# Optimization experiments

Hardware: AMD Instinct MI355X
Metric: run time of the kernel (lower is better)

Reference implementation:

```python
import jax, jax.numpy as jnp
import numpy as np

TOKEN_DIM = 256
NUM_HEADS = 2
IN_DIMS = 512
D = TOKEN_DIM * NUM_HEADS  # 512
SCALE = TOKEN_DIM ** (-0.5)


def _l2norm(v, axis):
    # torch F.normalize: v / max(||v||_2, eps)
    n = jnp.sqrt(jnp.sum(v * v, axis=axis, keepdims=True))
    return v / jnp.maximum(n, 1e-12)


def setup_inputs() -> dict:
    key = jax.random.key(0)
    ks = jax.random.split(key, 10)
    b, n = 8, 4096
    x = jax.random.normal(ks[0], (b, n, IN_DIMS), dtype=jnp.float32)
    s = 0.02
    Wq = jax.random.normal(ks[1], (IN_DIMS, D), dtype=jnp.float32) * s
    bq = jax.random.normal(ks[2], (D,), dtype=jnp.float32) * s
    Wk = jax.random.normal(ks[3], (IN_DIMS, D), dtype=jnp.float32) * s
    bk = jax.random.normal(ks[4], (D,), dtype=jnp.float32) * s
    Wr = jax.random.normal(ks[5], (D, TOKEN_DIM), dtype=jnp.float32) * s
    br = jax.random.normal(ks[6], (TOKEN_DIM,), dtype=jnp.float32) * s
    w_alpha = jax.random.normal(ks[7], (D, 1), dtype=jnp.float32)
    w_beta = jax.random.normal(ks[8], (D, 1), dtype=jnp.float32)
    return {"x": x, "Wq": Wq, "bq": bq, "Wk": Wk, "bk": bk,
            "Wr": Wr, "br": br, "w_alpha": w_alpha, "w_beta": w_beta}


def reference(x, Wq, bq, Wk, bk, Wr, br, w_alpha, w_beta):
    # x: [b, n, in_dims]
    q = x @ Wq + bq                      # [b, n, D]
    k = x @ Wk + bk                      # [b, n, D]
    q = _l2norm(q, axis=-1)
    k = _l2norm(k, axis=-1)
    v = _l2norm(k, axis=-1)              # original bug: value = normalize(key)

    alpha_w = (q @ w_alpha) * SCALE      # [b, n, 1]
    alpha_w = _l2norm(alpha_w, axis=1)   # normalize over token axis
    g_q = jnp.sum(alpha_w * q, axis=1)   # [b, D]
    g_q = jax.nn.softmax(g_q, axis=-1)

    p = g_q[:, None, :] * k              # [b, n, D]
    beta_w = _l2norm((p @ w_beta) * SCALE, axis=1)  # [b, n, 1]
    g_k = jnp.sum(beta_w * p, axis=1)    # [b, D]
    g_k = jax.nn.softmax(g_k, axis=-1)

    kvi = g_k[:, None, :] * v + q        # [b, n, D]
    return kvi @ Wr + br                 # [b, n, token_dim]
```

## Files before the change

kernel.cpp:

```cpp
#include <hip/hip_runtime.h>
#include <hip/hip_bf16.h>
#include <stdint.h>

#define BATCH    8
#define NTOKB    4096
#define NTOK     (BATCH * NTOKB)
#define DIN      512
#define DD       512
#define TD       256
#define SCALE    0.0625f
#define LSTR     36

typedef unsigned short ushortT;
typedef __attribute__((ext_vector_type(8))) short  short8;
typedef __attribute__((ext_vector_type(4))) float  f32x4;

union Frag { uint4 u; short8 s; };

__device__ __forceinline__ float bf_lo(uint32_t u) { return __uint_as_float(u << 16); }
__device__ __forceinline__ float bf_hi(uint32_t u) { return __uint_as_float(u & 0xffff0000u); }
__device__ __forceinline__ ushortT f2bf(float f) {
    uint32_t u = __float_as_uint(f);
    return (ushortT)((u + 0x7fffu + ((u >> 16) & 1u)) >> 16);
}
__device__ __forceinline__ short8 lds_frag(const ushortT* p) {
    uint2 a = *reinterpret_cast<const uint2*>(p);
    uint2 b = *reinterpret_cast<const uint2*>(p + 4);
    Frag f; f.u.x = a.x; f.u.y = a.y; f.u.z = b.x; f.u.w = b.y;
    return f.s;
}
__device__ __forceinline__ void gload_lds16(const ushortT* g, ushortT* l) {
    __builtin_amdgcn_global_load_lds(
        (const __attribute__((address_space(1))) uint32_t*)(const void*)g,
        (__attribute__((address_space(3))) uint32_t*)(void*)l,
        16, 0, 0);
}

__global__ __launch_bounds__(256) void packw_kernel(
    const float* __restrict__ Wq, const float* __restrict__ Wk,
    const float* __restrict__ Wr, ushortT* __restrict__ W16)
{
    const int blk = blockIdx.x;
    if (blk < 32) {
        const int mat = blk >> 4, c = blk & 15;
        const float* S = mat ? Wk : Wq;
        ushortT* D = W16 + (size_t)mat * (512 * 512) + (size_t)c * 16384;
        for (int i = threadIdx.x; i < 16384; i += 256) {
            int n = i & 511, p = i >> 9;
            int l = ((p >> 3) ^ ((n >> 1) & 3)) * 8 + (p & 7);
            D[n * 32 + p] = f2bf(S[(size_t)(c * 32 + l) * 512 + n]);
        }
    } else {
        const int c = blk - 32;
        ushortT* D = W16 + (size_t)2 * (512 * 512) + (size_t)c * 8192;
        for (int i = threadIdx.x; i < 8192; i += 256) {
            int n = i & 255, p = i >> 8;
            int l = ((p >> 3) ^ ((n >> 1) & 3)) * 8 + (p & 7);
            D[n * 32 + p] = f2bf(Wr[(size_t)(c * 32 + l) * 256 + n]);
        }
    }
}

__global__ __launch_bounds__(512) void gemm_qk_kernel(
    const float* __restrict__ x, const ushortT* __restrict__ W16,
    const float* __restrict__ bq, const float* __restrict__ bk,
    const float* __restrict__ w_alpha,
    ushortT* __restrict__ qn, ushortT* __restrict__ kn,
    float* __restrict__ alpha_raw, float* __restrict__ gq_raw)
{
    __shared__ __align__(16) ushortT xs[64 * LSTR];
    __shared__ __align__(16) ushortT wsd[512 * 32];
    __shared__ float rowsq[8][64];
    __shared__ float alphap[8][64];
    __shared__ float rnorm_s[64];
    __shared__ float alpha_sh[64];

    const int tid = threadIdx.x;
    const int mat = blockIdx.y;
    const size_t tok0 = (size_t)blockIdx.x * 64;
    const int b = (int)(blockIdx.x >> 6);
    const ushortT* Wb = W16 + (size_t)mat * (512 * 512);
    const float* bias = mat ? bk : bq;
    ushortT* dst = mat ? kn : qn;

    const int lane = tid & 63, w = tid >> 6;
    const int m = lane & 15, quad = lane >> 4;

    f32x4 acc[4][4];
    #pragma unroll
    for (int tr = 0; tr < 4; ++tr)
        #pragma unroll
        for (int tc = 0; tc < 4; ++tc) acc[tr][tc] = (f32x4){0.f, 0.f, 0.f, 0.f};

    const int xtok = tid >> 3;
    const int xkg  = (tid & 7) * 4;
    const float* xsrc = x + (tok0 + xtok) * DIN;

    for (int c = 0; c < 16; ++c) {
        __syncthreads();
        {
            float4 xv = *reinterpret_cast<const float4*>(xsrc + c * 32 + xkg);
            ushort4 xb;
            xb.x = f2bf(xv.x); xb.y = f2bf(xv.y); xb.z = f2bf(xv.z); xb.w = f2bf(xv.w);
            *reinterpret_cast<ushort4*>(&xs[xtok * LSTR + xkg]) = xb;
        }
        {
            const ushortT* wsrc = Wb + (size_t)c * 16384;
            #pragma unroll
            for (int i = 0; i < 4; ++i) {
                const int region = i * 8 + w;
                gload_lds16(wsrc + region * 512 + lane * 8, &wsd[region * 512]);
            }
        }
        __syncthreads();
        {
            short8 af[4], bfv[4];
            #pragma unroll
            for (int tr = 0; tr < 4; ++tr)
                af[tr] = lds_frag(&xs[(tr * 16 + m) * LSTR + quad * 8]);
            #pragma unroll
            for (int tc = 0; tc < 4; ++tc) {
                const int n = w * 64 + tc * 16 + m;
                bfv[tc] = *reinterpret_cast<const short8*>(
                    &wsd[n * 32 + ((quad ^ ((n >> 1) & 3)) * 8)]);
            }
            #pragma unroll
            for (int tr = 0; tr < 4; ++tr)
                #pragma unroll
                for (int tc = 0; tc < 4; ++tc)
                    acc[tr][tc] = __builtin_amdgcn_mfma_f32_16x16x32_bf16(af[tr], bfv[tc], acc[tr][tc], 0, 0, 0);
        }
    }

    float biasv[4], wa[4];
    #pragma unroll
    for (int tc = 0; tc < 4; ++tc) {
        biasv[tc] = bias[w * 64 + tc * 16 + m];
        wa[tc] = (mat == 0) ? w_alpha[w * 64 + tc * 16 + m] : 0.f;
    }
    #pragma unroll
    for (int tr = 0; tr < 4; ++tr)
        #pragma unroll
        for (int tc = 0; tc < 4; ++tc)
            #pragma unroll
            for (int reg = 0; reg < 4; ++reg)
                acc[tr][tc][reg] += biasv[tc];

    __syncthreads();
    #pragma unroll
    for (int tr = 0; tr < 4; ++tr) {
        #pragma unroll
        for (int reg = 0; reg < 4; ++reg) {
            float s = 0.f, a = 0.f;
            #pragma unroll
            for (int tc = 0; tc < 4; ++tc) {
                float v = acc[tr][tc][reg];
                s = fmaf(v, v, s);
                a = fmaf(v, wa[tc], a);
            }
            #pragma unroll
            for (int off = 1; off < 16; off <<= 1) {
                s += __shfl_xor(s, off);
                a += __shfl_xor(a, off);
            }
            if (m == 0) {
                rowsq[w][tr * 16 + quad * 4 + reg] = s;
                alphap[w][tr * 16 + quad * 4 + reg] = a;
            }
        }
    }
    __syncthreads();
    if (tid < 64) {
        float ss = 0.f, aa = 0.f;
        #pragma unroll
        for (int w2 = 0; w2 < 8; ++w2) { ss += rowsq[w2][tid]; aa += alphap[w2][tid]; }
        float rn = 1.0f / fmaxf(sqrtf(ss), 1e-12f);
        float av = SCALE * aa * rn;
        rnorm_s[tid] = rn;
        alpha_sh[tid] = av;
        if (mat == 0) alpha_raw[tok0 + tid] = av;
    }
    __syncthreads();
    float gqp[4] = {0.f, 0.f, 0.f, 0.f};
    #pragma unroll
    for (int tr = 0; tr < 4; ++tr) {
        #pragma unroll
        for (int reg = 0; reg < 4; ++reg) {
            const int rloc = tr * 16 + quad * 4 + reg;
            float rn = rnorm_s[rloc];
            float av = alpha_sh[rloc];
            size_t row = tok0 + rloc;
            ushortT* rp = dst + row * DD + w * 64 + m;
            #pragma unroll
            for (int tc = 0; tc < 4; ++tc) {
                float val = acc[tr][tc][reg] * rn;
                rp[tc * 16] = f2bf(val);
                gqp[tc] = fmaf(av, val, gqp[tc]);
            }
        }
    }
    if (mat == 0) {
        #pragma unroll
        for (int tc = 0; tc < 4; ++tc) {
            float p = gqp[tc];
            p += __shfl_xor(p, 16);
            p += __shfl_xor(p, 32);
            if (quad == 0)
                atomicAdd(&gq_raw[b * DD + w * 64 + tc * 16 + m], p);
        }
    }
}

__global__ __launch_bounds__(256) void fused_softmax_kernel(
    const float* __restrict__ nrm_in, const float* __restrict__ in,
    const float* __restrict__ mul, const float* __restrict__ wbeta,
    float* __restrict__ out, float* __restrict__ wb2)
{
    int b = blockIdx.x, tid = threadIdx.x;
    __shared__ float red[256];
    float s = 0.f;
    for (int i = tid; i < NTOKB; i += 256) {
        float v = nrm_in[b * NTOKB + i];
        s = fmaf(v, v, s);
    }
    red[tid] = s;
    __syncthreads();
    for (int off = 128; off > 0; off >>= 1) {
        if (tid < off) red[tid] += red[tid + off];
        __syncthreads();
    }
    float inv = 1.0f / fmaxf(sqrtf(red[0]), 1e-12f);
    __syncthreads();
    float v0 = in[b * DD + tid] * inv, v1 = in[b * DD + 256 + tid] * inv;
    if (mul) { v0 *= mul[b * DD + tid]; v1 *= mul[b * DD + 256 + tid]; }
    red[tid] = fmaxf(v0, v1);
    __syncthreads();
    for (int off = 128; off > 0; off >>= 1) {
        if (tid < off) red[tid] = fmaxf(red[tid], red[tid + off]);
        __syncthreads();
    }
    float m = red[0];
    __syncthreads();
    float e0 = expf(v0 - m), e1 = expf(v1 - m);
    red[tid] = e0 + e1;
    __syncthreads();
    for (int off = 128; off > 0; off >>= 1) {
        if (tid < off) red[tid] += red[tid + off];
        __syncthreads();
    }
    float rs = 1.0f / red[0];
    float o0 = e0 * rs, o1 = e1 * rs;
    out[b * DD + tid] = o0;
    out[b * DD + 256 + tid] = o1;
    if (wb2) {
        wb2[b * DD + tid]       = o0 * wbeta[tid];
        wb2[b * DD + 256 + tid] = o1 * wbeta[256 + tid];
    }
}

__global__ __launch_bounds__(256) void betawsum_kernel(
    const ushortT* __restrict__ kn, const float* __restrict__ wb2,
    float* __restrict__ beta_raw, float* __restrict__ h_raw)
{
    const int blk = blockIdx.x, tid = threadIdx.x;
    const int b = blk >> 6;
    const int i0 = (blk & 63) * 64;
    __shared__ float bs[64];

    const int wave = tid >> 6, lane = tid & 63;
    float4 wv0 = *reinterpret_cast<const float4*>(wb2 + b * DD + lane * 8);
    float4 wv1 = *reinterpret_cast<const float4*>(wb2 + b * DD + lane * 8 + 4);

    for (int it = 0; it < 16; ++it) {
        const int t = it * 4 + wave;
        const size_t tok = (size_t)b * NTOKB + i0 + t;
        uint4 kv = *reinterpret_cast<const uint4*>(kn + tok * DD + lane * 8);
        float s = bf_lo(kv.x) * wv0.x + bf_hi(kv.x) * wv0.y
                + bf_lo(kv.y) * wv0.z + bf_hi(kv.y) * wv0.w
                + bf_lo(kv.z) * wv1.x + bf_hi(kv.z) * wv1.y
                + bf_lo(kv.w) * wv1.z + bf_hi(kv.w) * wv1.w;
        #pragma unroll
        for (int off = 32; off > 0; off >>= 1) s += __shfl_xor(s, off);
        if (lane == 0) {
            float bv = SCALE * s;
            bs[t] = bv;
            beta_raw[tok] = bv;
        }
    }
    __syncthreads();

    const uint32_t* M32 = reinterpret_cast<const uint32_t*>(kn);
    size_t base = ((size_t)b * NTOKB + i0) * 256 + tid;
    float a0 = 0.f, a1 = 0.f;
    for (int ii = 0; ii < 64; ++ii) {
        uint32_t v = M32[base + (size_t)ii * 256];
        float wv = bs[ii];
        a0 = fmaf(wv, bf_lo(v), a0);
        a1 = fmaf(wv, bf_hi(v), a1);
    }
    atomicAdd(&h_raw[b * DD + 2 * tid],     a0);
    atomicAdd(&h_raw[b * DD + 2 * tid + 1], a1);
}

__global__ __launch_bounds__(256) void out_mfma_kernel(
    const ushortT* __restrict__ qn, const ushortT* __restrict__ kn,
    const float* __restrict__ g_k, const ushortT* __restrict__ WrT,
    const float* __restrict__ br, float* __restrict__ out)
{
    __shared__ __align__(16) ushortT kvs[64 * LSTR];
    __shared__ __align__(16) ushortT wrs[256 * 32];
    __shared__ float gks[512];

    const int tid = threadIdx.x;
    const size_t tok0 = (size_t)blockIdx.x * 64;
    const int b = (int)(tok0 >> 12);

    gks[tid] = g_k[b * DD + tid];
    gks[256 + tid] = g_k[b * DD + 256 + tid];

    const int lane = tid & 63, w = tid >> 6;
    const int m = lane & 15, quad = lane >> 4;

    f32x4 acc[4][4];
    #pragma unroll
    for (int tr = 0; tr < 4; ++tr)
        #pragma unroll
        for (int tc = 0; tc < 4; ++tc) acc[tr][tc] = (f32x4){0.f, 0.f, 0.f, 0.f};

    const int st  = tid >> 2;
    const int skg = (tid & 3) * 8;

    for (int c = 0; c < 16; ++c) {
        __syncthreads();
        {
            const size_t base = (tok0 + st) * DD + c * 32 + skg;
            uint4 qv = *reinterpret_cast<const uint4*>(qn + base);
            uint4 kv = *reinterpret_cast<const uint4*>(kn + base);
            const float* g = &gks[c * 32 + skg];
            ushortT o[8];
            o[0] = f2bf(fmaf(g[0], bf_lo(kv.x), bf_lo(qv.x)));
            o[1] = f2bf(fmaf(g[1], bf_hi(kv.x), bf_hi(qv.x)));
            o[2] = f2bf(fmaf(g[2], bf_lo(kv.y), bf_lo(qv.y)));
            o[3] = f2bf(fmaf(g[3], bf_hi(kv.y), bf_hi(qv.y)));
            o[4] = f2bf(fmaf(g[4], bf_lo(kv.z), bf_lo(qv.z)));
            o[5] = f2bf(fmaf(g[5], bf_hi(kv.z), bf_hi(qv.z)));
            o[6] = f2bf(fmaf(g[6], bf_lo(kv.w), bf_lo(qv.w)));
            o[7] = f2bf(fmaf(g[7], bf_hi(kv.w), bf_hi(qv.w)));
            uint2* lp = reinterpret_cast<uint2*>(&kvs[st * LSTR + skg]);
            lp[0] = make_uint2(((uint32_t)o[1] << 16) | o[0], ((uint32_t)o[3] << 16) | o[2]);
            lp[1] = make_uint2(((uint32_t)o[5] << 16) | o[4], ((uint32_t)o[7] << 16) | o[6]);
        }
        {
            const ushortT* wsrc = WrT + (size_t)c * 8192;
            #pragma unroll
            for (int i = 0; i < 4; ++i) {
                const int region = i * 4 + w;
                gload_lds16(wsrc + region * 512 + lane * 8, &wrs[region * 512]);
            }
        }
        __syncthreads();
        {
            short8 af[4], bfr[4];
            #pragma unroll
            for (int tr = 0; tr < 4; ++tr)
                af[tr] = lds_frag(&kvs[(tr * 16 + m) * LSTR + quad * 8]);
            #pragma unroll
            for (int tc = 0; tc < 4; ++tc) {
                const int n = w * 64 + tc * 16 + m;
                bfr[tc] = *reinterpret_cast<const short8*>(
                    &wrs[n * 32 + ((quad ^ ((n >> 1) & 3)) * 8)]);
            }
            #pragma unroll
            for (int tr = 0; tr < 4; ++tr)
                #pragma unroll
                for (int tc = 0; tc < 4; ++tc)
                    acc[tr][tc] = __builtin_amdgcn_mfma_f32_16x16x32_bf16(af[tr], bfr[tc], acc[tr][tc], 0, 0, 0);
        }
    }

    float brv[4];
    #pragma unroll
    for (int tc = 0; tc < 4; ++tc) brv[tc] = br[w * 64 + tc * 16 + m];
    #pragma unroll
    for (int tr = 0; tr < 4; ++tr) {
        #pragma unroll
        for (int reg = 0; reg < 4; ++reg) {
            size_t row = tok0 + tr * 16 + quad * 4 + reg;
            float* rp = out + row * TD + w * 64 + m;
            #pragma unroll
            for (int tc = 0; tc < 4; ++tc)
                rp[tc * 16] = acc[tr][tc][reg] + brv[tc];
        }
    }
}

extern "C" void kernel_launch(void* const* d_in, const int* in_sizes, int n_in,
                              void* d_out, int out_size, void* d_ws, size_t ws_size,
                              hipStream_t stream)
{
    const float* x       = (const float*)d_in[0];
    const float* Wq      = (const float*)d_in[1];
    const float* bq      = (const float*)d_in[2];
    const float* Wk      = (const float*)d_in[3];
    const float* bk      = (const float*)d_in[4];
    const float* Wr      = (const float*)d_in[5];
    const float* br      = (const float*)d_in[6];
    const float* w_alpha = (const float*)d_in[7];
    const float* w_beta  = (const float*)d_in[8];
    float* out = (float*)d_out;

    ushortT* kn = (ushortT*)d_out;

    char* ws = (char*)d_ws;
    ushortT* qn = (ushortT*)ws;        ws += (size_t)NTOK * DD * sizeof(ushortT);
    ushortT* W16 = (ushortT*)ws;       ws += (size_t)2 * 512 * 512 * sizeof(ushortT)
                                           + (size_t)512 * 256 * sizeof(ushortT);
    float* alpha_raw = (float*)ws;     ws += (size_t)NTOK * sizeof(float);
    float* beta_raw  = (float*)ws;     ws += (size_t)NTOK * sizeof(float);
    float* gq_raw = (float*)ws;        ws += (size_t)BATCH * DD * sizeof(float);
    float* h_raw  = (float*)ws;        ws += (size_t)BATCH * DD * sizeof(float);
    float* g_q    = (float*)ws;        ws += (size_t)BATCH * DD * sizeof(float);
    float* wb2    = (float*)ws;        ws += (size_t)BATCH * DD * sizeof(float);
    float* g_k    = (float*)ws;        ws += (size_t)BATCH * DD * sizeof(float);
    ushortT* WrT = W16 + (size_t)2 * 512 * 512;

    hipMemsetAsync(gq_raw, 0, 2 * BATCH * DD * sizeof(float), stream);

    packw_kernel<<<48, 256, 0, stream>>>(Wq, Wk, Wr, W16);
    gemm_qk_kernel<<<dim3(NTOK / 64, 2), 512, 0, stream>>>(x, W16, bq, bk, w_alpha,
                                                           qn, kn, alpha_raw, gq_raw);
    fused_softmax_kernel<<<BATCH, 256, 0, stream>>>(alpha_raw, gq_raw, nullptr,
                                                    w_beta, g_q, wb2);
    betawsum_kernel<<<NTOK / 64, 256, 0, stream>>>(kn, wb2, beta_raw, h_raw);
    fused_softmax_kernel<<<BATCH, 256, 0, stream>>>(beta_raw, h_raw, g_q,
                                                    nullptr, g_k, nullptr);
    out_mfma_kernel<<<NTOK / 64, 256, 0, stream>>>(qn, kn, g_k, WrT, br, out);
}
```

Measured before the change: 232.6 us.

## Fold g_k scaling into per-batch Wr copy and run two MFMA GEMMs

```diff
diff --git a/kernel.cpp b/kernel.cpp
--- a/kernel.cpp
+++ b/kernel.cpp
@@ -214,10 +214,13 @@
 __global__ __launch_bounds__(256) void fused_softmax_kernel(
     const float* __restrict__ nrm_in, const float* __restrict__ in,
     const float* __restrict__ mul, const float* __restrict__ wbeta,
-    float* __restrict__ out, float* __restrict__ wb2)
+    const float* __restrict__ Wr_orig,
+    float* __restrict__ out, float* __restrict__ wb2,
+    ushortT* __restrict__ Wrg)
 {
     int b = blockIdx.x, tid = threadIdx.x;
     __shared__ float red[256];
+    __shared__ float g_sh[512];
     float s = 0.f;
     for (int i = tid; i < NTOKB; i += 256) {
         float v = nrm_in[b * NTOKB + i];
@@ -255,6 +258,25 @@
     if (wb2) {
         wb2[b * DD + tid]       = o0 * wbeta[tid];
         wb2[b * DD + 256 + tid] = o1 * wbeta[256 + tid];
+    }
+    if (Wrg) {
+        g_sh[tid] = o0; g_sh[256 + tid] = o1;
+        __syncthreads();
+        const int n = tid;
+        ushortT* Db = Wrg + (size_t)b * (512 * 256);
+        for (int c = 0; c < 16; ++c) {
+            __align__(16) ushortT ov[32];
+            #pragma unroll
+            for (int p = 0; p < 32; ++p) {
+                int l = ((p >> 3) ^ ((n >> 1) & 3)) * 8 + (p & 7);
+                int k = c * 32 + l;
+                ov[p] = f2bf(g_sh[k] * Wr_orig[(size_t)k * TD + n]);
+            }
+            uint4* dst4 = reinterpret_cast<uint4*>(Db + (size_t)c * 8192 + (size_t)n * 32);
+            const uint4* src4 = reinterpret_cast<const uint4*>(ov);
+            dst4[0] = src4[0]; dst4[1] = src4[1];
+            dst4[2] = src4[2]; dst4[3] = src4[3];
+        }
     }
 }
 
@@ -304,19 +326,17 @@
 
 __global__ __launch_bounds__(256) void out_mfma_kernel(
     const ushortT* __restrict__ qn, const ushortT* __restrict__ kn,
-    const float* __restrict__ g_k, const ushortT* __restrict__ WrT,
+    const ushortT* __restrict__ WrT, const ushortT* __restrict__ Wrg,
     const float* __restrict__ br, float* __restrict__ out)
 {
-    __shared__ __align__(16) ushortT kvs[64 * LSTR];
-    __shared__ __align__(16) ushortT wrs[256 * 32];
-    __shared__ float gks[512];
+    __shared__ __align__(16) ushortT qs[64 * LSTR];
+    __shared__ __align__(16) ushortT ks[64 * LSTR];
+    __shared__ __align__(16) ushortT wrs[2 * 256 * 32];
 
     const int tid = threadIdx.x;
     const size_t tok0 = (size_t)blockIdx.x * 64;
     const int b = (int)(tok0 >> 12);
-
-    gks[tid] = g_k[b * DD + tid];
-    gks[256 + tid] = g_k[b * DD + 256 + tid];
+    const ushortT* Wgb = Wrg + (size_t)b * (512 * 256);
 
     const int lane = tid & 63, w = tid >> 6;
     const int m = lane & 15, quad = lane >> 4;
@@ -336,45 +356,45 @@
             const size_t base = (tok0 + st) * DD + c * 32 + skg;
             uint4 qv = *reinterpret_cast<const uint4*>(qn + base);
             uint4 kv = *reinterpret_cast<const uint4*>(kn + base);
-            const float* g = &gks[c * 32 + skg];
-            ushortT o[8];
-            o[0] = f2bf(fmaf(g[0], bf_lo(kv.x), bf_lo(qv.x)));
-            o[1] = f2bf(fmaf(g[1], bf_hi(kv.x), bf_hi(qv.x)));
-            o[2] = f2bf(fmaf(g[2], bf_lo(kv.y), bf_lo(qv.y)));
-            o[3] = f2bf(fmaf(g[3], bf_hi(kv.y), bf_hi(qv.y)));
-            o[4] = f2bf(fmaf(g[4], bf_lo(kv.z), bf_lo(qv.z)));
-            o[5] = f2bf(fmaf(g[5], bf_hi(kv.z), bf_hi(qv.z)));
-            o[6] = f2bf(fmaf(g[6], bf_lo(kv.w), bf_lo(qv.w)));
-            o[7] = f2bf(fmaf(g[7], bf_hi(kv.w), bf_hi(qv.w)));
-            uint2* lp = reinterpret_cast<uint2*>(&kvs[st * LSTR + skg]);
-            lp[0] = make_uint2(((uint32_t)o[1] << 16) | o[0], ((uint32_t)o[3] << 16) | o[2]);
-            lp[1] = make_uint2(((uint32_t)o[5] << 16) | o[4], ((uint32_t)o[7] << 16) | o[6]);
+            uint2* lq = reinterpret_cast<uint2*>(&qs[st * LSTR + skg]);
+            lq[0] = make_uint2(qv.x, qv.y);
+            lq[1] = make_uint2(qv.z, qv.w);
+            uint2* lk = reinterpret_cast<uint2*>(&ks[st * LSTR + skg]);
+            lk[0] = make_uint2(kv.x, kv.y);
+            lk[1] = make_uint2(kv.z, kv.w);
         }
         {
             const ushortT* wsrc = WrT + (size_t)c * 8192;
+            const ushortT* gsrc = Wgb + (size_t)c * 8192;
             #pragma unroll
             for (int i = 0; i < 4; ++i) {
                 const int region = i * 4 + w;
                 gload_lds16(wsrc + region * 512 + lane * 8, &wrs[region * 512]);
-            }
-        }
-        __syncthreads();
-        {
-            short8 af[4], bfr[4];
-            #pragma unroll
-            for (int tr = 0; tr < 4; ++tr)
-                af[tr] = lds_frag(&kvs[(tr * 16 + m) * LSTR + quad * 8]);
+                gload_lds16(gsrc + region * 512 + lane * 8, &wrs[8192 + region * 512]);
+            }
+        }
+        __syncthreads();
+        {
+            short8 aq[4], ak[4], br_[4], bg[4];
+            #pragma unroll
+            for (int tr = 0; tr < 4; ++tr) {
+                aq[tr] = lds_frag(&qs[(tr * 16 + m) * LSTR + quad * 8]);
+                ak[tr] = lds_frag(&ks[(tr * 16 + m) * LSTR + quad * 8]);
+            }
             #pragma unroll
             for (int tc = 0; tc < 4; ++tc) {
                 const int n = w * 64 + tc * 16 + m;
-                bfr[tc] = *reinterpret_cast<const short8*>(
-                    &wrs[n * 32 + ((quad ^ ((n >> 1) & 3)) * 8)]);
+                const int off = n * 32 + ((quad ^ ((n >> 1) & 3)) * 8);
+                br_[tc] = *reinterpret_cast<const short8*>(&wrs[off]);
+                bg[tc]  = *reinterpret_cast<const short8*>(&wrs[8192 + off]);
             }
             #pragma unroll
             for (int tr = 0; tr < 4; ++tr)
                 #pragma unroll
-                for (int tc = 0; tc < 4; ++tc)
-                    acc[tr][tc] = __builtin_amdgcn_mfma_f32_16x16x32_bf16(af[tr], bfr[tc], acc[tr][tc], 0, 0, 0);
+                for (int tc = 0; tc < 4; ++tc) {
+                    acc[tr][tc] = __builtin_amdgcn_mfma_f32_16x16x32_bf16(aq[tr], br_[tc], acc[tr][tc], 0, 0, 0);
+                    acc[tr][tc] = __builtin_amdgcn_mfma_f32_16x16x32_bf16(ak[tr], bg[tc],  acc[tr][tc], 0, 0, 0);
+                }
         }
     }
 
@@ -415,6 +435,7 @@
     ushortT* qn = (ushortT*)ws;        ws += (size_t)NTOK * DD * sizeof(ushortT);
     ushortT* W16 = (ushortT*)ws;       ws += (size_t)2 * 512 * 512 * sizeof(ushortT)
                                            + (size_t)512 * 256 * sizeof(ushortT);
+    ushortT* Wrg = (ushortT*)ws;       ws += (size_t)BATCH * 512 * 256 * sizeof(ushortT);
     float* alpha_raw = (float*)ws;     ws += (size_t)NTOK * sizeof(float);
     float* beta_raw  = (float*)ws;     ws += (size_t)NTOK * sizeof(float);
     float* gq_raw = (float*)ws;        ws += (size_t)BATCH * DD * sizeof(float);
@@ -430,9 +451,9 @@
     gemm_qk_kernel<<<dim3(NTOK / 64, 2), 512, 0, stream>>>(x, W16, bq, bk, w_alpha,
                                                            qn, kn, alpha_raw, gq_raw);
     fused_softmax_kernel<<<BATCH, 256, 0, stream>>>(alpha_raw, gq_raw, nullptr,
-                                                    w_beta, g_q, wb2);
+                                                    w_beta, nullptr, g_q, wb2, nullptr);
     betawsum_kernel<<<NTOK / 64, 256, 0, stream>>>(kn, wb2, beta_raw, h_raw);
     fused_softmax_kernel<<<BATCH, 256, 0, stream>>>(beta_raw, h_raw, g_q,
-                                                    nullptr, g_k, nullptr);
-    out_mfma_kernel<<<NTOK / 64, 256, 0, stream>>>(qn, kn, g_k, WrT, br, out);
-}
+                                                    nullptr, Wr, g_k, nullptr, Wrg);
+    out_mfma_kernel<<<NTOK / 64, 256, 0, stream>>>(qn, kn, WrT, Wrg, br, out);
+}
```

Measured after the change: 338.2 us. 1.45x slower.

## Double-buffer x and W tiles in the QK GEMM main loop

Applied to the files above, without the earlier changes.

```diff
diff --git a/kernel.cpp b/kernel.cpp
--- a/kernel.cpp
+++ b/kernel.cpp
@@ -68,8 +68,8 @@
     ushortT* __restrict__ qn, ushortT* __restrict__ kn,
     float* __restrict__ alpha_raw, float* __restrict__ gq_raw)
 {
-    __shared__ __align__(16) ushortT xs[64 * LSTR];
-    __shared__ __align__(16) ushortT wsd[512 * 32];
+    __shared__ __align__(16) ushortT xs[2][64 * LSTR];
+    __shared__ __align__(16) ushortT wsd[2][512 * 32];
     __shared__ float rowsq[8][64];
     __shared__ float alphap[8][64];
     __shared__ float rnorm_s[64];
@@ -96,40 +96,63 @@
     const int xkg  = (tid & 7) * 4;
     const float* xsrc = x + (tok0 + xtok) * DIN;
 
+    {
+        float4 xv = *reinterpret_cast<const float4*>(xsrc + xkg);
+        const ushortT* wsrc = Wb;
+        #pragma unroll
+        for (int i = 0; i < 4; ++i) {
+            const int region = i * 8 + w;
+            gload_lds16(wsrc + region * 512 + lane * 8, &wsd[0][region * 512]);
+        }
+        ushort4 xb;
+        xb.x = f2bf(xv.x); xb.y = f2bf(xv.y); xb.z = f2bf(xv.z); xb.w = f2bf(xv.w);
+        *reinterpret_cast<ushort4*>(&xs[0][xtok * LSTR + xkg]) = xb;
+    }
+    asm volatile("s_waitcnt lgkmcnt(0)" ::: "memory");
+    __builtin_amdgcn_s_barrier();
+
     for (int c = 0; c < 16; ++c) {
-        __syncthreads();
-        {
-            float4 xv = *reinterpret_cast<const float4*>(xsrc + c * 32 + xkg);
-            ushort4 xb;
-            xb.x = f2bf(xv.x); xb.y = f2bf(xv.y); xb.z = f2bf(xv.z); xb.w = f2bf(xv.w);
-            *reinterpret_cast<ushort4*>(&xs[xtok * LSTR + xkg]) = xb;
-        }
-        {
-            const ushortT* wsrc = Wb + (size_t)c * 16384;
+        const int cur = c & 1, nxt = cur ^ 1;
+        float4 xv;
+        if (c < 15) {
+            xv = *reinterpret_cast<const float4*>(xsrc + (c + 1) * 32 + xkg);
+            const ushortT* wsrc = Wb + (size_t)(c + 1) * 16384;
             #pragma unroll
             for (int i = 0; i < 4; ++i) {
                 const int region = i * 8 + w;
-                gload_lds16(wsrc + region * 512 + lane * 8, &wsd[region * 512]);
-            }
-        }
-        __syncthreads();
+                gload_lds16(wsrc + region * 512 + lane * 8, &wsd[nxt][region * 512]);
+            }
+            asm volatile("s_waitcnt vmcnt(5)" ::: "memory");
+        } else {
+            asm volatile("s_waitcnt vmcnt(0)" ::: "memory");
+        }
+        __builtin_amdgcn_s_barrier();
         {
             short8 af[4], bfv[4];
             #pragma unroll
             for (int tr = 0; tr < 4; ++tr)
-                af[tr] = lds_frag(&xs[(tr * 16 + m) * LSTR + quad * 8]);
+                af[tr] = lds_frag(&xs[cur][(tr * 16 + m) * LSTR + quad * 8]);
             #pragma unroll
             for (int tc = 0; tc < 4; ++tc) {
                 const int n = w * 64 + tc * 16 + m;
                 bfv[tc] = *reinterpret_cast<const short8*>(
-                    &wsd[n * 32 + ((quad ^ ((n >> 1) & 3)) * 8)]);
-            }
+                    &wsd[cur][n * 32 + ((quad ^ ((n >> 1) & 3)) * 8)]);
+            }
+            __builtin_amdgcn_s_setprio(1);
             #pragma unroll
             for (int tr = 0; tr < 4; ++tr)
                 #pragma unroll
                 for (int tc = 0; tc < 4; ++tc)
                     acc[tr][tc] = __builtin_amdgcn_mfma_f32_16x16x32_bf16(af[tr], bfv[tc], acc[tr][tc], 0, 0, 0);
-        }
+            __builtin_amdgcn_s_setprio(0);
+        }
+        if (c < 15) {
+            ushort4 xb;
+            xb.x = f2bf(xv.x); xb.y = f2bf(xv.y); xb.z = f2bf(xv.z); xb.w = f2bf(xv.w);
+            *reinterpret_cast<ushort4*>(&xs[nxt][xtok * LSTR + xkg]) = xb;
+        }
+        asm volatile("s_waitcnt lgkmcnt(0)" ::: "memory");
+        __builtin_amdgcn_s_barrier();
     }
 
     float biasv[4], wa[4];
```

After: 244.2 us. +5.0%, slower.
